# Kernel optimization log

Measured on AMD Instinct MI355X. Metric: run time of the kernel, lower is better.

## Reference

```python
import jax, jax.numpy as jnp
import numpy as np

NEG_INF = 1e10  # module's self.inf


def setup_inputs() -> dict:
    key = jax.random.key(0)
    k1, k2, k3, k4 = jax.random.split(key, 4)
    B, To, Ti, d = 16, 2048, 2048, 64
    q = jax.random.normal(k1, (B, To, d), dtype=jnp.float32)
    k = jax.random.normal(k2, (B, Ti, d), dtype=jnp.float32)
    v = jax.random.normal(k3, (B, Ti, d), dtype=jnp.float32)
    prod_mask = jax.random.randint(k4, (B, To, Ti), 0, 2, dtype=jnp.int32)
    return {"q": q, "k": k, "v": v, "prod_mask": prod_mask}


def reference(q, k, v, prod_mask):
    d_qk = q.shape[2]
    # [B, To, Ti] scores
    scaled_qk = jnp.einsum('bod,bid->boi', q, k) / jnp.sqrt(jnp.float32(d_qk))
    scaled_qk = jnp.where(prod_mask == 0, jnp.float32(-NEG_INF), scaled_qk)
    weights = jax.nn.softmax(scaled_qk, axis=2)
    # v flattened over trailing dims is already [B, Ti, d] here
    attended_v = jnp.einsum('boi,bid->bod', weights, v)
    return attended_v
```

## Files before the change

kernel.cpp:

```cpp
#include <hip/hip_runtime.h>
#include <stdint.h>

#define BATCH 16
#define TO 2048
#define TI 2048
#define DH 64
#define NITER (TI / 64)

typedef __attribute__((ext_vector_type(8))) short bf16x8;
typedef __attribute__((ext_vector_type(4))) float f32x4;

__device__ __forceinline__ unsigned short f2bf(float f) {
  uint32_t x = __float_as_uint(f);
  x += 0x7fffu + ((x >> 16) & 1u);
  return (unsigned short)(x >> 16);
}

__global__ __launch_bounds__(256) void convert_kv(
    const float* __restrict__ kg, const float* __restrict__ vg,
    unsigned short* __restrict__ k_bf, unsigned short* __restrict__ v_t) {
  __shared__ __align__(16) unsigned short vt[64][72];
  int b = blockIdx.y;
  int i0 = blockIdx.x * 64;
  int t = threadIdx.x;

  {
    const float4* src = (const float4*)(kg + ((size_t)b * TI + i0) * DH);
    ushort4* dst = (ushort4*)(k_bf + ((size_t)b * TI + i0) * DH);
#pragma unroll
    for (int u = 0; u < 4; ++u) {
      float4 f = src[t + 256 * u];
      ushort4 o;
      o.x = f2bf(f.x); o.y = f2bf(f.y); o.z = f2bf(f.z); o.w = f2bf(f.w);
      dst[t + 256 * u] = o;
    }
  }
  {
    const float4* src = (const float4*)(vg + ((size_t)b * TI + i0) * DH);
#pragma unroll
    for (int u = 0; u < 4; ++u) {
      int idx = t + 256 * u;
      int row = idx >> 4;
      int c4 = idx & 15;
      float4 f = src[idx];
      vt[c4 * 4 + 0][row] = f2bf(f.x);
      vt[c4 * 4 + 1][row] = f2bf(f.y);
      vt[c4 * 4 + 2][row] = f2bf(f.z);
      vt[c4 * 4 + 3][row] = f2bf(f.w);
    }
  }
  __syncthreads();
  {
    int dd = t >> 2, part = t & 3;
    ushort4* dst = (ushort4*)(v_t + ((size_t)b * DH + dd) * TI + i0 + part * 16);
#pragma unroll
    for (int u = 0; u < 4; ++u) {
      ushort4 o;
      o.x = vt[dd][part * 16 + u * 4 + 0];
      o.y = vt[dd][part * 16 + u * 4 + 1];
      o.z = vt[dd][part * 16 + u * 4 + 2];
      o.w = vt[dd][part * 16 + u * 4 + 3];
      dst[u] = o;
    }
  }
}

__global__ __launch_bounds__(256) void attn_kernel(
    const float* __restrict__ q, const int* __restrict__ mask,
    const unsigned short* __restrict__ k_bf, const unsigned short* __restrict__ v_t,
    float* __restrict__ out) {
  __shared__ __align__(16) unsigned short k_lds[2][64][72];
  __shared__ __align__(16) unsigned short v_lds[2][64][72];
  __shared__ __align__(16) unsigned short p_row[4][16][72];

  int b = blockIdx.y;
  int o_blk = blockIdx.x;
  int t = threadIdx.x;
  int wave = t >> 6;
  int lane = t & 63;
  int ln15 = lane & 15;
  int quad = lane >> 4;

  int o0 = o_blk * 64 + wave * 16;
  int qrow = o0 + ln15;

  bf16x8 qf[2];
  {
    const float* qp = q + ((size_t)b * TO + qrow) * DH;
#pragma unroll
    for (int kc = 0; kc < 2; ++kc) {
      int kk = kc * 32 + quad * 8;
      float4 f0 = *(const float4*)(qp + kk);
      float4 f1 = *(const float4*)(qp + kk + 4);
      bf16x8 a;
      a[0] = (short)f2bf(f0.x * 0.125f);
      a[1] = (short)f2bf(f0.y * 0.125f);
      a[2] = (short)f2bf(f0.z * 0.125f);
      a[3] = (short)f2bf(f0.w * 0.125f);
      a[4] = (short)f2bf(f1.x * 0.125f);
      a[5] = (short)f2bf(f1.y * 0.125f);
      a[6] = (short)f2bf(f1.z * 0.125f);
      a[7] = (short)f2bf(f1.w * 0.125f);
      qf[kc] = a;
    }
  }

  f32x4 o_acc[4];
#pragma unroll
  for (int dt = 0; dt < 4; ++dt) o_acc[dt] = (f32x4){0.f, 0.f, 0.f, 0.f};
  float l_part = 0.f;

  int row = t >> 2, part = t & 3;
  const uint4* kp = (const uint4*)(k_bf + ((size_t)b * TI + row) * DH + part * 16);
  const uint4* vp = (const uint4*)(v_t + ((size_t)b * DH + row) * TI + part * 16);
  const int* mbase = mask + ((size_t)b * TO + qrow) * TI + quad * 4;

  uint4 ka0 = kp[0], ka1 = kp[1];
  uint4 va0 = vp[0], va1 = vp[1];
  kp = (const uint4*)((const char*)kp + 64 * DH * 2);
  vp = (const uint4*)((const char*)vp + 64 * 2);
  *(uint4*)&k_lds[0][row][part * 16] = ka0;
  *(uint4*)&k_lds[0][row][part * 16 + 8] = ka1;
  *(uint4*)&v_lds[0][row][part * 16] = va0;
  *(uint4*)&v_lds[0][row][part * 16 + 8] = va1;
  ka0 = kp[0]; ka1 = kp[1];
  va0 = vp[0]; va1 = vp[1];
  kp = (const uint4*)((const char*)kp + 64 * DH * 2);
  vp = (const uint4*)((const char*)vp + 64 * 2);
  int4 mv[4];
#pragma unroll
  for (int mt = 0; mt < 4; ++mt) mv[mt] = *(const int4*)(mbase + mt * 16);
  mbase += 64;
  __syncthreads();

  for (int ic = 0; ic < NITER; ++ic) {
    int cur = ic & 1;

    int4 mnext[4];
    if (ic < NITER - 1) {
#pragma unroll
      for (int mt = 0; mt < 4; ++mt) mnext[mt] = *(const int4*)(mbase + mt * 16);
      mbase += 64;
    }

    if (ic < NITER - 1) {
      *(uint4*)&k_lds[cur ^ 1][row][part * 16] = ka0;
      *(uint4*)&k_lds[cur ^ 1][row][part * 16 + 8] = ka1;
      *(uint4*)&v_lds[cur ^ 1][row][part * 16] = va0;
      *(uint4*)&v_lds[cur ^ 1][row][part * 16 + 8] = va1;
    }
    if (ic < NITER - 2) {
      ka0 = kp[0]; ka1 = kp[1];
      va0 = vp[0]; va1 = vp[1];
      kp = (const uint4*)((const char*)kp + 64 * DH * 2);
      vp = (const uint4*)((const char*)vp + 64 * 2);
    }

    f32x4 st[4];
#pragma unroll
    for (int mt = 0; mt < 4; ++mt) {
      bf16x8 kf0 = *(const bf16x8*)&k_lds[cur][mt * 16 + ln15][quad * 8];
      bf16x8 kf1 = *(const bf16x8*)&k_lds[cur][mt * 16 + ln15][32 + quad * 8];
      f32x4 acc = (f32x4){0.f, 0.f, 0.f, 0.f};
      acc = __builtin_amdgcn_mfma_f32_16x16x32_bf16(kf0, qf[0], acc, 0, 0, 0);
      acc = __builtin_amdgcn_mfma_f32_16x16x32_bf16(kf1, qf[1], acc, 0, 0, 0);
      st[mt] = acc;
    }

#pragma unroll
    for (int mt = 0; mt < 4; ++mt) {
      float p0 = (mv[mt].x != 0) ? __expf(st[mt][0]) : 0.f;
      float p1 = (mv[mt].y != 0) ? __expf(st[mt][1]) : 0.f;
      float p2 = (mv[mt].z != 0) ? __expf(st[mt][2]) : 0.f;
      float p3 = (mv[mt].w != 0) ? __expf(st[mt][3]) : 0.f;
      l_part += (p0 + p1) + (p2 + p3);
      uint32_t lo = (uint32_t)f2bf(p0) | ((uint32_t)f2bf(p1) << 16);
      uint32_t hi = (uint32_t)f2bf(p2) | ((uint32_t)f2bf(p3) << 16);
      uint2 pk; pk.x = lo; pk.y = hi;
      *(uint2*)&p_row[wave][ln15][mt * 16 + quad * 4] = pk;
    }
#pragma unroll
    for (int mt = 0; mt < 4; ++mt) mv[mt] = mnext[mt];

    bf16x8 pf0 = *(const bf16x8*)&p_row[wave][ln15][quad * 8];
    bf16x8 pf1 = *(const bf16x8*)&p_row[wave][ln15][32 + quad * 8];

#pragma unroll
    for (int dt = 0; dt < 4; ++dt) {
      bf16x8 vf0 = *(const bf16x8*)&v_lds[cur][dt * 16 + ln15][quad * 8];
      bf16x8 vf1 = *(const bf16x8*)&v_lds[cur][dt * 16 + ln15][32 + quad * 8];
      o_acc[dt] = __builtin_amdgcn_mfma_f32_16x16x32_bf16(vf0, pf0, o_acc[dt], 0, 0, 0);
      o_acc[dt] = __builtin_amdgcn_mfma_f32_16x16x32_bf16(vf1, pf1, o_acc[dt], 0, 0, 0);
    }

    __syncthreads();
  }

  l_part += __shfl_xor(l_part, 16);
  l_part += __shfl_xor(l_part, 32);
  float inv = 1.0f / l_part;
  float* orow = out + ((size_t)b * TO + qrow) * DH;
#pragma unroll
  for (int dt = 0; dt < 4; ++dt) {
    float4 vout;
    vout.x = o_acc[dt][0] * inv;
    vout.y = o_acc[dt][1] * inv;
    vout.z = o_acc[dt][2] * inv;
    vout.w = o_acc[dt][3] * inv;
    *(float4*)(orow + dt * 16 + quad * 4) = vout;
  }
}

extern "C" void kernel_launch(void* const* d_in, const int* in_sizes, int n_in,
                              void* d_out, int out_size, void* d_ws, size_t ws_size,
                              hipStream_t stream) {
  const float* q = (const float*)d_in[0];
  const float* k = (const float*)d_in[1];
  const float* v = (const float*)d_in[2];
  const int* mask = (const int*)d_in[3];

  unsigned short* k_bf = (unsigned short*)d_ws;
  unsigned short* v_t = k_bf + (size_t)BATCH * TI * DH;

  convert_kv<<<dim3(TI / 64, BATCH), 256, 0, stream>>>(k, v, k_bf, v_t);
  attn_kernel<<<dim3(TO / 64, BATCH), 256, 0, stream>>>(q, mask, k_bf, v_t, (float*)d_out);
}
```

Measured before the change: 79.45 us.

## Remap blocks to XCDs by batch, unroll loop by two, lighten barrier

The launch grid becomes 1D, and the block index is remapped so that each of the 8 XCDs handles two batches. The blocks on one XCD then share the same K/V data in that XCD's L2. The main loop is manually unrolled by two with compile-time LDS buffer indices, and mask registers ping-pong between two arrays, which removes the copy of the mask registers each iteration. __syncthreads is replaced by an inline s_waitcnt lgkmcnt(0) plus s_barrier that does not wait on outstanding global loads, so the K/V/mask prefetches can stay in flight across the barrier. The manual barrier relies on the compiler placing vmcnt waits correctly before the prefetched registers are used.

```diff
diff --git a/kernel.cpp b/kernel.cpp
--- a/kernel.cpp
+++ b/kernel.cpp
@@ -65,6 +65,61 @@
   }
 }
 
+#define ATTN_BODY(CUR, IC, MCUR, MNXT)                                         \
+  {                                                                            \
+    if ((IC) < NITER - 1) {                                                    \
+      _Pragma("unroll") for (int mt = 0; mt < 4; ++mt)                         \
+          MNXT[mt] = *(const int4*)(mbase + mt * 16);                          \
+      mbase += 64;                                                             \
+         \
+      *(uint4*)&k_lds[(CUR) ^ 1][row][part * 16] = ka0;                        \
+      *(uint4*)&k_lds[(CUR) ^ 1][row][part * 16 + 8] = ka1;                    \
+      *(uint4*)&v_lds[(CUR) ^ 1][row][part * 16] = va0;                        \
+      *(uint4*)&v_lds[(CUR) ^ 1][row][part * 16 + 8] = va1;                    \
+    }                                                                          \
+        \
+    if ((IC) < NITER - 2) {                                                    \
+      ka0 = kp[0]; ka1 = kp[1];                                                \
+      va0 = vp[0]; va1 = vp[1];                                                \
+      kp = (const uint4*)((const char*)kp + 64 * DH * 2);                      \
+      vp = (const uint4*)((const char*)vp + 64 * 2);                           \
+    }                                                                          \
+                                                  \
+    f32x4 st[4];                                                               \
+    _Pragma("unroll") for (int mt = 0; mt < 4; ++mt) {                         \
+      bf16x8 kf0 = *(const bf16x8*)&k_lds[CUR][mt * 16 + ln15][quad * 8];      \
+      bf16x8 kf1 = *(const bf16x8*)&k_lds[CUR][mt * 16 + ln15][32 + quad * 8]; \
+      f32x4 acc = (f32x4){0.f, 0.f, 0.f, 0.f};                                 \
+      acc = __builtin_amdgcn_mfma_f32_16x16x32_bf16(kf0, qf[0], acc, 0, 0, 0); \
+      acc = __builtin_amdgcn_mfma_f32_16x16x32_bf16(kf1, qf[1], acc, 0, 0, 0); \
+      st[mt] = acc;                                                            \
+    }                                                                          \
+         \
+    _Pragma("unroll") for (int mt = 0; mt < 4; ++mt) {                         \
+      float p0 = (MCUR[mt].x != 0) ? __expf(st[mt][0]) : 0.f;                  \
+      float p1 = (MCUR[mt].y != 0) ? __expf(st[mt][1]) : 0.f;                  \
+      float p2 = (MCUR[mt].z != 0) ? __expf(st[mt][2]) : 0.f;                  \
+      float p3 = (MCUR[mt].w != 0) ? __expf(st[mt][3]) : 0.f;                  \
+      l_part += (p0 + p1) + (p2 + p3);                                         \
+      uint32_t lo = (uint32_t)f2bf(p0) | ((uint32_t)f2bf(p1) << 16);           \
+      uint32_t hi = (uint32_t)f2bf(p2) | ((uint32_t)f2bf(p3) << 16);           \
+      uint2 pk; pk.x = lo; pk.y = hi;                                          \
+      *(uint2*)&p_row[wave][ln15][mt * 16 + quad * 4] = pk;                    \
+    }                                                                          \
+            \
+    bf16x8 pf0 = *(const bf16x8*)&p_row[wave][ln15][quad * 8];                 \
+    bf16x8 pf1 = *(const bf16x8*)&p_row[wave][ln15][32 + quad * 8];            \
+                                             \
+    _Pragma("unroll") for (int dt = 0; dt < 4; ++dt) {                         \
+      bf16x8 vf0 = *(const bf16x8*)&v_lds[CUR][dt * 16 + ln15][quad * 8];      \
+      bf16x8 vf1 = *(const bf16x8*)&v_lds[CUR][dt * 16 + ln15][32 + quad * 8]; \
+      o_acc[dt] = __builtin_amdgcn_mfma_f32_16x16x32_bf16(vf0, pf0, o_acc[dt], 0, 0, 0); \
+      o_acc[dt] = __builtin_amdgcn_mfma_f32_16x16x32_bf16(vf1, pf1, o_acc[dt], 0, 0, 0); \
+    }                                                                          \
+          \
+    asm volatile("s_waitcnt lgkmcnt(0)\n\ts_barrier" ::: "memory");            \
+  }
+
 __global__ __launch_bounds__(256) void attn_kernel(
     const float* __restrict__ q, const int* __restrict__ mask,
     const unsigned short* __restrict__ k_bf, const unsigned short* __restrict__ v_t,
@@ -73,8 +128,12 @@
   __shared__ __align__(16) unsigned short v_lds[2][64][72];
   __shared__ __align__(16) unsigned short p_row[4][16][72];
 
-  int b = blockIdx.y;
-  int o_blk = blockIdx.x;
+  int n = blockIdx.x;
+  int xcd = n & 7;
+  int slot = n >> 3;
+  int b = (xcd << 1) | (slot >> 5);
+  int o_blk = slot & 31;
+
   int t = threadIdx.x;
   int wave = t >> 6;
   int lane = t & 63;
@@ -127,73 +186,15 @@
   va0 = vp[0]; va1 = vp[1];
   kp = (const uint4*)((const char*)kp + 64 * DH * 2);
   vp = (const uint4*)((const char*)vp + 64 * 2);
-  int4 mv[4];
+  int4 mv[4], mw[4];
 #pragma unroll
   for (int mt = 0; mt < 4; ++mt) mv[mt] = *(const int4*)(mbase + mt * 16);
   mbase += 64;
-  __syncthreads();
-
-  for (int ic = 0; ic < NITER; ++ic) {
-    int cur = ic & 1;
-
-    int4 mnext[4];
-    if (ic < NITER - 1) {
-#pragma unroll
-      for (int mt = 0; mt < 4; ++mt) mnext[mt] = *(const int4*)(mbase + mt * 16);
-      mbase += 64;
-    }
-
-    if (ic < NITER - 1) {
-      *(uint4*)&k_lds[cur ^ 1][row][part * 16] = ka0;
-      *(uint4*)&k_lds[cur ^ 1][row][part * 16 + 8] = ka1;
-      *(uint4*)&v_lds[cur ^ 1][row][part * 16] = va0;
-      *(uint4*)&v_lds[cur ^ 1][row][part * 16 + 8] = va1;
-    }
-    if (ic < NITER - 2) {
-      ka0 = kp[0]; ka1 = kp[1];
-      va0 = vp[0]; va1 = vp[1];
-      kp = (const uint4*)((const char*)kp + 64 * DH * 2);
-      vp = (const uint4*)((const char*)vp + 64 * 2);
-    }
-
-    f32x4 st[4];
-#pragma unroll
-    for (int mt = 0; mt < 4; ++mt) {
-      bf16x8 kf0 = *(const bf16x8*)&k_lds[cur][mt * 16 + ln15][quad * 8];
-      bf16x8 kf1 = *(const bf16x8*)&k_lds[cur][mt * 16 + ln15][32 + quad * 8];
-      f32x4 acc = (f32x4){0.f, 0.f, 0.f, 0.f};
-      acc = __builtin_amdgcn_mfma_f32_16x16x32_bf16(kf0, qf[0], acc, 0, 0, 0);
-      acc = __builtin_amdgcn_mfma_f32_16x16x32_bf16(kf1, qf[1], acc, 0, 0, 0);
-      st[mt] = acc;
-    }
-
-#pragma unroll
-    for (int mt = 0; mt < 4; ++mt) {
-      float p0 = (mv[mt].x != 0) ? __expf(st[mt][0]) : 0.f;
-      float p1 = (mv[mt].y != 0) ? __expf(st[mt][1]) : 0.f;
-      float p2 = (mv[mt].z != 0) ? __expf(st[mt][2]) : 0.f;
-      float p3 = (mv[mt].w != 0) ? __expf(st[mt][3]) : 0.f;
-      l_part += (p0 + p1) + (p2 + p3);
-      uint32_t lo = (uint32_t)f2bf(p0) | ((uint32_t)f2bf(p1) << 16);
-      uint32_t hi = (uint32_t)f2bf(p2) | ((uint32_t)f2bf(p3) << 16);
-      uint2 pk; pk.x = lo; pk.y = hi;
-      *(uint2*)&p_row[wave][ln15][mt * 16 + quad * 4] = pk;
-    }
-#pragma unroll
-    for (int mt = 0; mt < 4; ++mt) mv[mt] = mnext[mt];
-
-    bf16x8 pf0 = *(const bf16x8*)&p_row[wave][ln15][quad * 8];
-    bf16x8 pf1 = *(const bf16x8*)&p_row[wave][ln15][32 + quad * 8];
-
-#pragma unroll
-    for (int dt = 0; dt < 4; ++dt) {
-      bf16x8 vf0 = *(const bf16x8*)&v_lds[cur][dt * 16 + ln15][quad * 8];
-      bf16x8 vf1 = *(const bf16x8*)&v_lds[cur][dt * 16 + ln15][32 + quad * 8];
-      o_acc[dt] = __builtin_amdgcn_mfma_f32_16x16x32_bf16(vf0, pf0, o_acc[dt], 0, 0, 0);
-      o_acc[dt] = __builtin_amdgcn_mfma_f32_16x16x32_bf16(vf1, pf1, o_acc[dt], 0, 0, 0);
-    }
-
-    __syncthreads();
+  asm volatile("s_waitcnt lgkmcnt(0)\n\ts_barrier" ::: "memory");
+
+  for (int ic = 0; ic < NITER; ic += 2) {
+    ATTN_BODY(0, ic, mv, mw)
+    ATTN_BODY(1, ic + 1, mw, mv)
   }
 
   l_part += __shfl_xor(l_part, 16);
@@ -223,5 +224,5 @@
   unsigned short* v_t = k_bf + (size_t)BATCH * TI * DH;
 
   convert_kv<<<dim3(TI / 64, BATCH), 256, 0, stream>>>(k, v, k_bf, v_t);
-  attn_kernel<<<dim3(TO / 64, BATCH), 256, 0, stream>>>(q, mask, k_bf, v_t, (float*)d_out);
-}
+  attn_kernel<<<dim3(TO / 64 * BATCH), 256, 0, stream>>>(q, mask, k_bf, v_t, (float*)d_out);
+}
```

New measurement: 77.57 us. 2.4% less time.
